# Kernel optimization log

Measured on AMD Instinct MI355X. Metric: run time of the kernel, lower is better.

Reference implementation:

```python
import jax, jax.numpy as jnp
import numpy as np

IN_V = 16
OUT_V = 16
HS = 64
INCR = 2
METRIC = jnp.array([1.0, -1.0, -1.0, -1.0], dtype=jnp.float32)


def setup_inputs() -> dict:
    key = jax.random.key(0)
    ks = jax.random.split(key, 9)
    B, N = 64, 1024
    vectors = jax.random.normal(ks[0], (B, N, IN_V, 4), dtype=jnp.float32)
    scalars = jax.random.normal(ks[1], (B, N, HS), dtype=jnp.float32)
    # kaiming-uniform-ish init scale for [out, in] weights
    def w(k, o, i):
        bound = 1.0 / np.sqrt(i)
        return jax.random.uniform(k, (o, i), jnp.float32, -bound, bound)
    Wq = w(ks[2], IN_V * INCR, IN_V)
    Wk = w(ks[3], IN_V * INCR, IN_V)
    Wv = w(ks[4], OUT_V, IN_V)  # exp() applied in forward (EquiLinearTimelike)
    Wq_s = w(ks[5], HS, HS)
    Wk_s = w(ks[6], HS, HS)
    bq_s = jax.random.uniform(ks[7], (HS,), jnp.float32, -1 / np.sqrt(HS), 1 / np.sqrt(HS))
    bk_s = jax.random.uniform(ks[8], (HS,), jnp.float32, -1 / np.sqrt(HS), 1 / np.sqrt(HS))
    return {"vectors": vectors, "scalars": scalars, "Wq": Wq, "Wq_s": Wq_s,
            "bq_s": bq_s, "Wk": Wk, "Wk_s": Wk_s, "bk_s": bk_s, "Wv": Wv}


def reference(vectors, scalars, Wq, Wq_s, bq_s, Wk, Wk_s, bk_s, Wv):
    B, N = vectors.shape[:2]
    # Lorentz squared norm: t^2 - x^2 - y^2 - z^2 over last axis -> [B,N,IN_V,1]
    norm = jnp.einsum('bnik,k->bni', vectors * vectors, METRIC)[..., None]
    vecs = vectors / jnp.sqrt(jnp.clip(jnp.abs(norm), 1e-5))
    # Q/K vector projections [B,N,IN_V*INCR,4] and scalar projections [B,N,HS]
    q_v = jnp.einsum('ij,bnjk->bnik', Wq, vecs)
    k_v = jnp.einsum('ij,bnjk->bnik', Wk, vecs)
    q_s = scalars @ Wq_s.T + bq_s
    k_s = scalars @ Wk_s.T + bk_s
    # embed: flatten vectors (K gets metric factor) and concat scalars
    q = jnp.concatenate([q_v.reshape(B, N, -1), q_s], axis=-1)
    k = jnp.concatenate([(k_v * METRIC).reshape(B, N, -1), k_s], axis=-1)
    # V: positive-weight (timelike) projection, flatten -> [B,N,OUT_V*4]
    v = jnp.einsum('ij,bnjk->bnik', jnp.exp(Wv), vecs).reshape(B, N, -1)
    # scaled dot-product attention over the particle axis
    scale = 1.0 / jnp.sqrt(jnp.asarray(q.shape[-1], q.dtype))
    scores = jnp.einsum('bqd,bkd->bqk', q, k) * scale
    attn = jax.nn.softmax(scores, axis=-1)
    out = jnp.einsum('bqk,bkd->bqd', attn, v)
    return out.reshape(B, N, -1, 4)
```

## Files before the change

kernel.cpp:

```cpp
#include <hip/hip_runtime.h>
#include <math.h>

typedef float f32x16 __attribute__((ext_vector_type(16)));
typedef short bf16x8 __attribute__((ext_vector_type(8)));
typedef short bf16x4 __attribute__((ext_vector_type(4)));
typedef unsigned short u16;
typedef unsigned int u32;

#define MFMA32(a, b, c) __builtin_amdgcn_mfma_f32_32x32x16_bf16(a, b, c, 0, 0, 0)

__device__ __forceinline__ u16 f2bf(float x) {
    u32 u = __float_as_uint(x);
    u += 0x7FFFu + ((u >> 16) & 1u);
    return (u16)(u >> 16);
}
__device__ __forceinline__ float bf2f(u16 h) {
    return __uint_as_float(((u32)h) << 16);
}
__device__ __forceinline__ void gload16(const void* g, void* l) {
    __builtin_amdgcn_global_load_lds(
        (const __attribute__((address_space(1))) unsigned int*)g,
        (__attribute__((address_space(3))) unsigned int*)l, 16, 0, 0);
}

__global__ __launch_bounds__(256) void g_kernel(
    const float* __restrict__ Wq, const float* __restrict__ Wk,
    const float* __restrict__ Wv,
    u16* __restrict__ gmh, u16* __restrict__ gml,
    u16* __restrict__ mvh, u16* __restrict__ mvl)
{
    const int bk = blockIdx.x;
    const int base = ((bk & 3) * 256 + threadIdx.x) * 4;
    if (bk < 4) {
#pragma unroll
        for (int i = 0; i < 4; ++i) {
            int e = base + i;
            int f = e >> 6, fp = e & 63;
            int c = f & 3, cp = fp & 3, j = f >> 2, jp = fp >> 2;
            float val = 0.f;
            if (c == cp) {
                float a0 = 0.f, a1 = 0.f;
#pragma unroll 8
                for (int ff = 0; ff < 32; ff += 2) {
                    a0 = fmaf(Wq[ff * 16 + j],       Wk[ff * 16 + jp],       a0);
                    a1 = fmaf(Wq[(ff + 1) * 16 + j], Wk[(ff + 1) * 16 + jp], a1);
                }
                val = (a0 + a1) * ((c == 0) ? 1.f : -1.f);
            }
            u16 h = f2bf(val);
            gmh[e] = h; gml[e] = f2bf(val - bf2f(h));
        }
    } else {
#pragma unroll
        for (int i = 0; i < 4; ++i) {
            int e = base + i;
            int f = e >> 6, fp = e & 63;
            float val = ((f & 3) == (fp & 3)) ? expf(Wv[(f >> 2) * 16 + (fp >> 2)]) : 0.f;
            u16 h = f2bf(val);
            mvh[e] = h; mvl[e] = f2bf(val - bf2f(h));
        }
    }
}

__global__ __launch_bounds__(256) void prep_kernel(
    const float* __restrict__ vectors, const float* __restrict__ scalars,
    const float* __restrict__ Wq_s, const float* __restrict__ bq_s,
    const float* __restrict__ Wk_s, const float* __restrict__ bk_s,
    const u16* __restrict__ gmh, const u16* __restrict__ gml,
    const u16* __restrict__ mvh, const u16* __restrict__ mvl,
    u16* __restrict__ qh, u16* __restrict__ ql,
    u16* __restrict__ kh, u16* __restrict__ kl,
    u16* __restrict__ vth)
{
    const int t = threadIdx.x;
    const int w = t >> 6;
    const int lane = t & 63;
    const int l31 = lane & 31, g = lane >> 5;
    const int b = blockIdx.x >> 5;
    const int n0 = (blockIdx.x & 31) << 5;
    const long tok0 = (long)b * 1024 + n0;
    const float SC2 = 0.07216878364870323f * 1.4426950408889634f;

    if (w == 1 || w == 2) {
        bf16x8 Ah[4], Al[4];
        const float* vrow = vectors + (tok0 + l31) * 64 + g * 8;
#pragma unroll
        for (int kk = 0; kk < 4; ++kk) {
            float4 x0 = *(const float4*)(vrow + kk * 16);
            float4 x1 = *(const float4*)(vrow + kk * 16 + 4);
            float nr0 = x0.x * x0.x - x0.y * x0.y - x0.z * x0.z - x0.w * x0.w;
            float iv0 = 1.0f / sqrtf(fmaxf(fabsf(nr0), 1e-5f));
            float nr1 = x1.x * x1.x - x1.y * x1.y - x1.z * x1.z - x1.w * x1.w;
            float iv1 = 1.0f / sqrtf(fmaxf(fabsf(nr1), 1e-5f));
            float xs[8] = {x0.x * iv0, x0.y * iv0, x0.z * iv0, x0.w * iv0,
                           x1.x * iv1, x1.y * iv1, x1.z * iv1, x1.w * iv1};
#pragma unroll
            for (int e = 0; e < 8; ++e) {
                u16 h = f2bf(xs[e]);
                Ah[kk][e] = (short)h;
                Al[kk][e] = (short)f2bf(xs[e] - bf2f(h));
            }
        }

        const u16* bhp = (w == 1) ? gmh : mvh;
        const u16* blp = (w == 1) ? gml : mvl;
#pragma unroll
        for (int tile = 0; tile < 2; ++tile) {
            const int fs = tile * 32 + l31;
            const u16* bh = bhp + fs * 64 + g * 8;
            const u16* bl = blp + fs * 64 + g * 8;
            f32x16 acc;
#pragma unroll
            for (int r = 0; r < 16; ++r) acc[r] = 0.f;
#pragma unroll
            for (int kk = 0; kk < 4; ++kk) {
                bf16x8 Bh = *(const bf16x8*)(bh + kk * 16);
                bf16x8 Bl = *(const bf16x8*)(bl + kk * 16);
                acc = MFMA32(Ah[kk], Bh, acc);
                acc = MFMA32(Al[kk], Bh, acc);
                acc = MFMA32(Ah[kk], Bl, acc);
            }
            if (w == 1) {
#pragma unroll
                for (int reg = 0; reg < 16; ++reg) {
                    int trow = (reg & 3) + 8 * (reg >> 2) + 4 * g;
                    float val = acc[reg];
                    u16 h = f2bf(val);
                    kh[(tok0 + trow) * 128 + fs] = h;
                    kl[(tok0 + trow) * 64 + fs] = f2bf(val - bf2f(h));
                }
            } else {
#pragma unroll
                for (int reg = 0; reg < 16; ++reg) {
                    int trow = (reg & 3) + 8 * (reg >> 2) + 4 * g;
                    vth[((long)b * 64 + fs) * 1024 + n0 + trow] = f2bf(acc[reg]);
                }
            }
        }
    } else {
        if (w == 0) {
            const float* vrow = vectors + (tok0 + l31) * 64 + g * 8;
#pragma unroll
            for (int kk = 0; kk < 4; ++kk) {
                float4 x0 = *(const float4*)(vrow + kk * 16);
                float4 x1 = *(const float4*)(vrow + kk * 16 + 4);
                float nr0 = x0.x * x0.x - x0.y * x0.y - x0.z * x0.z - x0.w * x0.w;
                float iv0 = SC2 / sqrtf(fmaxf(fabsf(nr0), 1e-5f));
                float nr1 = x1.x * x1.x - x1.y * x1.y - x1.z * x1.z - x1.w * x1.w;
                float iv1 = SC2 / sqrtf(fmaxf(fabsf(nr1), 1e-5f));
                float xs[8] = {x0.x * iv0, x0.y * iv0, x0.z * iv0, x0.w * iv0,
                               x1.x * iv1, x1.y * iv1, x1.z * iv1, x1.w * iv1};
                u16 hh[8], ll[8];
#pragma unroll
                for (int e = 0; e < 8; ++e) {
                    hh[e] = f2bf(xs[e]);
                    ll[e] = f2bf(xs[e] - bf2f(hh[e]));
                }
                *(int4*)(qh + (tok0 + l31) * 128 + kk * 16 + g * 8) = *(int4*)hh;
                *(int4*)(ql + (tok0 + l31) * 64 + kk * 16 + g * 8) = *(int4*)ll;
            }
        }
        const int isq = (w == 0);
        bf16x8 Ah[4];
        const float* xrow = scalars + (tok0 + l31) * 64 + g * 8;
#pragma unroll
        for (int kk = 0; kk < 4; ++kk) {
            float4 x0 = *(const float4*)(xrow + kk * 16);
            float4 x1 = *(const float4*)(xrow + kk * 16 + 4);
            float xs[8] = {x0.x, x0.y, x0.z, x0.w, x1.x, x1.y, x1.z, x1.w};
#pragma unroll
            for (int e = 0; e < 8; ++e) Ah[kk][e] = (short)f2bf(xs[e]);
        }
        const float sc = isq ? SC2 : 1.f;
        u16* oh = isq ? qh : kh;
#pragma unroll
        for (int ft = 0; ft < 2; ++ft) {
            const int fs = (ft << 5) + l31;
            const float* wrow = (isq ? Wq_s : Wk_s) + fs * 64 + g * 8;
            f32x16 acc;
#pragma unroll
            for (int r = 0; r < 16; ++r) acc[r] = 0.f;
#pragma unroll
            for (int kk = 0; kk < 4; ++kk) {
                float4 w0_ = *(const float4*)(wrow + kk * 16);
                float4 w1_ = *(const float4*)(wrow + kk * 16 + 4);
                float ws_[8] = {w0_.x, w0_.y, w0_.z, w0_.w, w1_.x, w1_.y, w1_.z, w1_.w};
                bf16x8 Bh;
#pragma unroll
                for (int e = 0; e < 8; ++e) Bh[e] = (short)f2bf(ws_[e]);
                acc = MFMA32(Ah[kk], Bh, acc);
            }
            const float bias = (isq ? bq_s : bk_s)[fs];
#pragma unroll
            for (int reg = 0; reg < 16; ++reg) {
                int trow = (reg & 3) + 8 * (reg >> 2) + 4 * g;
                oh[(tok0 + trow) * 128 + 64 + fs] = f2bf((acc[reg] + bias) * sc);
            }
        }
    }
}

__global__ __launch_bounds__(256) void attn_kernel(
    const u16* __restrict__ qh, const u16* __restrict__ ql,
    const u16* __restrict__ kh, const u16* __restrict__ kl,
    const u16* __restrict__ vth, float* __restrict__ out)
{
    __shared__ u16 KH[2 * 32 * 128];
    __shared__ u16 KL[2 * 32 * 64];
    __shared__ u16 VH[2 * 64 * 40];

    const int t = threadIdx.x;
    const int lane = t & 63;
    const int w = t >> 6;
    const int l31 = lane & 31, g = lane >> 5;

    const int bid = blockIdx.x;
    const int b = ((bid & 7) << 3) + (bid >> 6);
    const int qt = (bid >> 3) & 7;

    const int qi = qt * 128 + w * 32 + l31;
    const long qtok = (long)b * 1024 + qi;

    bf16x8 Qh[8], Qlv[4];
    {
        const u16* qhp = qh + qtok * 128 + g * 8;
        const u16* qlp = ql + qtok * 64 + g * 8;
#pragma unroll
        for (int c = 0; c < 8; ++c) Qh[c] = *(const bf16x8*)(qhp + c * 16);
#pragma unroll
        for (int c = 0; c < 4; ++c) Qlv[c] = *(const bf16x8*)(qlp + c * 16);
    }

    const int r0 = 8 * w + (lane >> 4);
    const int r1 = r0 + 4;
    const int su0 = (lane & 15) ^ (r0 & 15);
    const int su1 = (lane & 15) ^ (r1 & 15);
    const u16* kh0 = kh + ((long)b * 1024 + r0) * 128 + su0 * 8;
    const u16* kh1 = kh + ((long)b * 1024 + r1) * 128 + su1 * 8;
    const int rl_ = 8 * w + (lane >> 3);
    const int sul = (lane & 7) ^ (rl_ & 7);
    const u16* kl0 = kl + ((long)b * 1024 + rl_) * 64 + sul * 8;

    const int vdv = t >> 2, vq4 = t & 3;
    const u16* vhg = vth + ((long)b * 64 + vdv) * 1024 + vq4 * 8;
    u16* vdst = VH + vdv * 40 + vq4 * 8;
    int4 rv0;

#define STAGEK(kt, bf) do { \
        gload16(kh0 + (long)(kt) * 128, KH + (bf) * 4096 + w * 1024); \
        gload16(kh1 + (long)(kt) * 128, KH + (bf) * 4096 + w * 1024 + 512); \
        gload16(kl0 + (long)(kt) * 64,  KL + (bf) * 2048 + w * 512); \
    } while (0)

    f32x16 o0, o1;
#pragma unroll
    for (int r = 0; r < 16; ++r) { o0[r] = 0.f; o1[r] = 0.f; }
    float m_run = -1e30f, l_run = 0.f;

    rv0 = *(const int4*)(vhg);
    STAGEK(0, 0);
    *(int4*)(vdst) = rv0;
    __syncthreads();

#pragma unroll 2
    for (int it = 0; it < 32; ++it) {
        const int cb = it & 1;
        if (it < 31) {
            rv0 = *(const int4*)(vhg + (it + 1) * 32);
            STAGEK((it + 1) * 32, cb ^ 1);
        }

        f32x16 sA, sB;
#pragma unroll
        for (int r = 0; r < 16; ++r) { sA[r] = 0.f; sB[r] = 0.f; }
        const u16* kbh = KH + cb * 4096 + l31 * 128;
        const u16* kbl = KL + cb * 2048 + l31 * 64;
        const int rs = l31 & 15, rs7 = l31 & 7;
        __builtin_amdgcn_s_setprio(1);
#pragma unroll
        for (int c = 0; c < 4; ++c) {
            bf16x8 fh = *(const bf16x8*)(kbh + ((g + 2 * c) ^ rs) * 8);
            bf16x8 fl = *(const bf16x8*)(kbl + ((g + 2 * c) ^ rs7) * 8);
            sA = MFMA32(fh, Qh[c], sA);
            sB = MFMA32(fl, Qh[c], sB);
            sB = MFMA32(fh, Qlv[c], sB);
        }
#pragma unroll
        for (int c = 4; c < 8; ++c) {
            bf16x8 fh = *(const bf16x8*)(kbh + ((g + 2 * c) ^ rs) * 8);
            sA = MFMA32(fh, Qh[c], sA);
        }
        __builtin_amdgcn_s_setprio(0);

        float s[16];
#pragma unroll
        for (int r = 0; r < 16; ++r) s[r] = sA[r] + sB[r];
        float m01 = fmaxf(s[0], s[1]),   m23 = fmaxf(s[2], s[3]);
        float m45 = fmaxf(s[4], s[5]),   m67 = fmaxf(s[6], s[7]);
        float m89 = fmaxf(s[8], s[9]),   mab = fmaxf(s[10], s[11]);
        float mcd = fmaxf(s[12], s[13]), mef = fmaxf(s[14], s[15]);
        float mt = fmaxf(fmaxf(fmaxf(m01, m23), fmaxf(m45, m67)),
                         fmaxf(fmaxf(m89, mab), fmaxf(mcd, mef)));
        mt = fmaxf(mt, __shfl_xor(mt, 32));
        if (!__all(mt - m_run <= 11.54f)) {
            float mn = fmaxf(m_run, mt);
            float corr = __builtin_amdgcn_exp2f(m_run - mn);
            l_run *= corr;
#pragma unroll
            for (int r = 0; r < 16; ++r) { o0[r] *= corr; o1[r] *= corr; }
            m_run = mn;
        }
#pragma unroll
        for (int r = 0; r < 16; ++r) s[r] = __builtin_amdgcn_exp2f(s[r] - m_run);
        float p01 = s[0] + s[1],   p23 = s[2] + s[3];
        float p45 = s[4] + s[5],   p67 = s[6] + s[7];
        float p89 = s[8] + s[9],   pab = s[10] + s[11];
        float pcd = s[12] + s[13], pef = s[14] + s[15];
        float ps = ((p01 + p23) + (p45 + p67)) + ((p89 + pab) + (pcd + pef));
        ps += __shfl_xor(ps, 32);
        l_run += ps;

        u32 pk[4], pk2[4];
#pragma unroll
        for (int e = 0; e < 4; ++e) {
            pk[e]  = __builtin_amdgcn_perm(__float_as_uint(s[2 * e + 1]),
                                           __float_as_uint(s[2 * e]), 0x07060302u);
            pk2[e] = __builtin_amdgcn_perm(__float_as_uint(s[8 + 2 * e + 1]),
                                           __float_as_uint(s[8 + 2 * e]), 0x07060302u);
        }
        bf16x8 ph0 = *(bf16x8*)pk;
        bf16x8 ph1 = *(bf16x8*)pk2;

        const u16* vb = VH + cb * 2560;
        bf16x8 v00, v01, v10, v11;
        {
            const u16* p00 = vb + l31 * 40 + g * 4;
            const u16* p10 = vb + (32 + l31) * 40 + g * 4;
            bf16x4 a0 = *(const bf16x4*)(p00);      bf16x4 a1 = *(const bf16x4*)(p00 + 8);
            bf16x4 b0 = *(const bf16x4*)(p00 + 16); bf16x4 b1 = *(const bf16x4*)(p00 + 24);
            bf16x4 c0 = *(const bf16x4*)(p10);      bf16x4 c1 = *(const bf16x4*)(p10 + 8);
            bf16x4 d0 = *(const bf16x4*)(p10 + 16); bf16x4 d1 = *(const bf16x4*)(p10 + 24);
            v00 = __builtin_shufflevector(a0, a1, 0, 1, 2, 3, 4, 5, 6, 7);
            v01 = __builtin_shufflevector(b0, b1, 0, 1, 2, 3, 4, 5, 6, 7);
            v10 = __builtin_shufflevector(c0, c1, 0, 1, 2, 3, 4, 5, 6, 7);
            v11 = __builtin_shufflevector(d0, d1, 0, 1, 2, 3, 4, 5, 6, 7);
        }

        __builtin_amdgcn_s_setprio(1);
        o0 = MFMA32(v00, ph0, o0);
        o0 = MFMA32(v01, ph1, o0);
        o1 = MFMA32(v10, ph0, o1);
        o1 = MFMA32(v11, ph1, o1);
        __builtin_amdgcn_s_setprio(0);

        if (it < 31) *(int4*)(vdst + (cb ^ 1) * 2560) = rv0;
        __syncthreads();
    }

    float inv = 1.0f / l_run;
    float* op = out + qtok * 64;
#pragma unroll
    for (int sg = 0; sg < 4; ++sg) {
        *(float4*)(op + sg * 8 + g * 4) = make_float4(
            o0[4*sg+0]*inv, o0[4*sg+1]*inv, o0[4*sg+2]*inv, o0[4*sg+3]*inv);
        *(float4*)(op + 32 + sg * 8 + g * 4) = make_float4(
            o1[4*sg+0]*inv, o1[4*sg+1]*inv, o1[4*sg+2]*inv, o1[4*sg+3]*inv);
    }
#undef STAGEK
}

extern "C" void kernel_launch(void* const* d_in, const int* in_sizes, int n_in,
                              void* d_out, int out_size, void* d_ws, size_t ws_size,
                              hipStream_t stream) {
    const float* vectors = (const float*)d_in[0];
    const float* scalars = (const float*)d_in[1];
    const float* Wq   = (const float*)d_in[2];
    const float* Wq_s = (const float*)d_in[3];
    const float* bq_s = (const float*)d_in[4];
    const float* Wk   = (const float*)d_in[5];
    const float* Wk_s = (const float*)d_in[6];
    const float* bk_s = (const float*)d_in[7];
    const float* Wv   = (const float*)d_in[8];
    float* o = (float*)d_out;

    u16* qh  = (u16*)d_ws;
    u16* ql  = qh + 8388608;
    u16* kh  = ql + 4194304;
    u16* kl  = kh + 8388608;
    u16* vth = kl + 4194304;
    u16* gmh = vth + 4194304;
    u16* gml = gmh + 4096;
    u16* mvh = gml + 4096;
    u16* mvl = mvh + 4096;

    g_kernel<<<8, 256, 0, stream>>>(Wq, Wk, Wv, gmh, gml, mvh, mvl);
    prep_kernel<<<2048, 256, 0, stream>>>(vectors, scalars, Wq_s, bq_s,
                                          Wk_s, bk_s, gmh, gml, mvh, mvl,
                                          qh, ql, kh, kl, vth);
    attn_kernel<<<512, 256, 0, stream>>>(qh, ql, kh, kl, vth, o);
}
```

Baseline: 92.55 us.

## Defer P·V MFMAs one iteration to overlap them with QK MFMAs

The P·V matrix multiplies of each KV tile are delayed by one iteration and issued right after the next tile's QK MFMAs, with a final flush after the loop. This keeps the matrix unit busy while the softmax VALU work and exp computation run, instead of serialising softmax and P·V. Accumulation order stays correct because the deferred product is added before the next running-max rescale. The cost is extra live registers for the carried V and P fragments, which may lower occupancy, plus one extra MFMA block on zeros in the first iteration.

Result: no change. 92.85 us (+0.3%).

```diff
diff --git a/kernel.cpp b/kernel.cpp
--- a/kernel.cpp
+++ b/kernel.cpp
@@ -257,6 +257,13 @@
     for (int r = 0; r < 16; ++r) { o0[r] = 0.f; o1[r] = 0.f; }
     float m_run = -1e30f, l_run = 0.f;
 
+    bf16x8 vp00, vp01, vp10, vp11, php0, php1;
+#pragma unroll
+    for (int e = 0; e < 8; ++e) {
+        vp00[e] = 0; vp01[e] = 0; vp10[e] = 0; vp11[e] = 0;
+        php0[e] = 0; php1[e] = 0;
+    }
+
     rv0 = *(const int4*)(vhg);
     STAGEK(0, 0);
     *(int4*)(vdst) = rv0;
@@ -290,6 +297,10 @@
             bf16x8 fh = *(const bf16x8*)(kbh + ((g + 2 * c) ^ rs) * 8);
             sA = MFMA32(fh, Qh[c], sA);
         }
+        o0 = MFMA32(vp00, php0, o0);
+        o0 = MFMA32(vp01, php1, o0);
+        o1 = MFMA32(vp10, php0, o1);
+        o1 = MFMA32(vp11, php1, o1);
         __builtin_amdgcn_s_setprio(0);
 
         float s[16];
@@ -328,11 +339,10 @@
             pk2[e] = __builtin_amdgcn_perm(__float_as_uint(s[8 + 2 * e + 1]),
                                            __float_as_uint(s[8 + 2 * e]), 0x07060302u);
         }
-        bf16x8 ph0 = *(bf16x8*)pk;
-        bf16x8 ph1 = *(bf16x8*)pk2;
+        php0 = *(bf16x8*)pk;
+        php1 = *(bf16x8*)pk2;
 
         const u16* vb = VH + cb * 2560;
-        bf16x8 v00, v01, v10, v11;
         {
             const u16* p00 = vb + l31 * 40 + g * 4;
             const u16* p10 = vb + (32 + l31) * 40 + g * 4;
@@ -340,22 +350,22 @@
             bf16x4 b0 = *(const bf16x4*)(p00 + 16); bf16x4 b1 = *(const bf16x4*)(p00 + 24);
             bf16x4 c0 = *(const bf16x4*)(p10);      bf16x4 c1 = *(const bf16x4*)(p10 + 8);
             bf16x4 d0 = *(const bf16x4*)(p10 + 16); bf16x4 d1 = *(const bf16x4*)(p10 + 24);
-            v00 = __builtin_shufflevector(a0, a1, 0, 1, 2, 3, 4, 5, 6, 7);
-            v01 = __builtin_shufflevector(b0, b1, 0, 1, 2, 3, 4, 5, 6, 7);
-            v10 = __builtin_shufflevector(c0, c1, 0, 1, 2, 3, 4, 5, 6, 7);
-            v11 = __builtin_shufflevector(d0, d1, 0, 1, 2, 3, 4, 5, 6, 7);
-        }
-
-        __builtin_amdgcn_s_setprio(1);
-        o0 = MFMA32(v00, ph0, o0);
-        o0 = MFMA32(v01, ph1, o0);
-        o1 = MFMA32(v10, ph0, o1);
-        o1 = MFMA32(v11, ph1, o1);
-        __builtin_amdgcn_s_setprio(0);
+            vp00 = __builtin_shufflevector(a0, a1, 0, 1, 2, 3, 4, 5, 6, 7);
+            vp01 = __builtin_shufflevector(b0, b1, 0, 1, 2, 3, 4, 5, 6, 7);
+            vp10 = __builtin_shufflevector(c0, c1, 0, 1, 2, 3, 4, 5, 6, 7);
+            vp11 = __builtin_shufflevector(d0, d1, 0, 1, 2, 3, 4, 5, 6, 7);
+        }
 
         if (it < 31) *(int4*)(vdst + (cb ^ 1) * 2560) = rv0;
         __syncthreads();
     }
+
+    __builtin_amdgcn_s_setprio(1);
+    o0 = MFMA32(vp00, php0, o0);
+    o0 = MFMA32(vp01, php1, o0);
+    o1 = MFMA32(vp10, php0, o1);
+    o1 = MFMA32(vp11, php1, o1);
+    __builtin_amdgcn_s_setprio(0);
 
     float inv = 1.0f / l_run;
     float* op = out + qtok * 64;
```

## Switch attention K/V staging to four-buffer ring with one barrier per two tiles

Applied to the files above, without the earlier changes.

Grows the shared-memory K/V staging from double to quadruple buffering and processes two 32-key tiles per loop step, prefetching the next two tiles ahead. This halves the number of __syncthreads barriers and gives global loads more time to land before use. The cost is doubled LDS footprint (about 64KB per block), which may cut occupancy, plus extra VGPRs for two register-held V prefetches.

After: 94.00 us. About the same (+1.6%).

```diff
diff --git a/kernel.cpp b/kernel.cpp
--- a/kernel.cpp
+++ b/kernel.cpp
@@ -205,9 +205,9 @@
     const u16* __restrict__ kh, const u16* __restrict__ kl,
     const u16* __restrict__ vth, float* __restrict__ out)
 {
-    __shared__ u16 KH[2 * 32 * 128];
-    __shared__ u16 KL[2 * 32 * 64];
-    __shared__ u16 VH[2 * 64 * 40];
+    __shared__ u16 KH[4 * 32 * 128];
+    __shared__ u16 KL[4 * 32 * 64];
+    __shared__ u16 VH[4 * 64 * 40];
 
     const int t = threadIdx.x;
     const int lane = t & 63;
@@ -244,7 +244,7 @@
     const int vdv = t >> 2, vq4 = t & 3;
     const u16* vhg = vth + ((long)b * 64 + vdv) * 1024 + vq4 * 8;
     u16* vdst = VH + vdv * 40 + vq4 * 8;
-    int4 rv0;
+    int4 rvA, rvB;
 
 #define STAGEK(kt, bf) do { \
         gload16(kh0 + (long)(kt) * 128, KH + (bf) * 4096 + w * 1024); \
@@ -257,103 +257,117 @@
     for (int r = 0; r < 16; ++r) { o0[r] = 0.f; o1[r] = 0.f; }
     float m_run = -1e30f, l_run = 0.f;
 
-    rv0 = *(const int4*)(vhg);
+    rvA = *(const int4*)(vhg);
+    rvB = *(const int4*)(vhg + 32);
     STAGEK(0, 0);
-    *(int4*)(vdst) = rv0;
+    STAGEK(32, 1);
+    *(int4*)(vdst) = rvA;
+    *(int4*)(vdst + 2560) = rvB;
+    rvA = *(const int4*)(vhg + 64);
+    rvB = *(const int4*)(vhg + 96);
     __syncthreads();
 
-#pragma unroll 2
-    for (int it = 0; it < 32; ++it) {
-        const int cb = it & 1;
-        if (it < 31) {
-            rv0 = *(const int4*)(vhg + (it + 1) * 32);
-            STAGEK((it + 1) * 32, cb ^ 1);
-        }
-
-        f32x16 sA, sB;
-#pragma unroll
-        for (int r = 0; r < 16; ++r) { sA[r] = 0.f; sB[r] = 0.f; }
-        const u16* kbh = KH + cb * 4096 + l31 * 128;
-        const u16* kbl = KL + cb * 2048 + l31 * 64;
-        const int rs = l31 & 15, rs7 = l31 & 7;
-        __builtin_amdgcn_s_setprio(1);
-#pragma unroll
-        for (int c = 0; c < 4; ++c) {
-            bf16x8 fh = *(const bf16x8*)(kbh + ((g + 2 * c) ^ rs) * 8);
-            bf16x8 fl = *(const bf16x8*)(kbl + ((g + 2 * c) ^ rs7) * 8);
-            sA = MFMA32(fh, Qh[c], sA);
-            sB = MFMA32(fl, Qh[c], sB);
-            sB = MFMA32(fh, Qlv[c], sB);
-        }
-#pragma unroll
-        for (int c = 4; c < 8; ++c) {
-            bf16x8 fh = *(const bf16x8*)(kbh + ((g + 2 * c) ^ rs) * 8);
-            sA = MFMA32(fh, Qh[c], sA);
-        }
-        __builtin_amdgcn_s_setprio(0);
-
-        float s[16];
-#pragma unroll
-        for (int r = 0; r < 16; ++r) s[r] = sA[r] + sB[r];
-        float m01 = fmaxf(s[0], s[1]),   m23 = fmaxf(s[2], s[3]);
-        float m45 = fmaxf(s[4], s[5]),   m67 = fmaxf(s[6], s[7]);
-        float m89 = fmaxf(s[8], s[9]),   mab = fmaxf(s[10], s[11]);
-        float mcd = fmaxf(s[12], s[13]), mef = fmaxf(s[14], s[15]);
-        float mt = fmaxf(fmaxf(fmaxf(m01, m23), fmaxf(m45, m67)),
-                         fmaxf(fmaxf(m89, mab), fmaxf(mcd, mef)));
-        mt = fmaxf(mt, __shfl_xor(mt, 32));
-        if (!__all(mt - m_run <= 11.54f)) {
-            float mn = fmaxf(m_run, mt);
-            float corr = __builtin_amdgcn_exp2f(m_run - mn);
-            l_run *= corr;
-#pragma unroll
-            for (int r = 0; r < 16; ++r) { o0[r] *= corr; o1[r] *= corr; }
-            m_run = mn;
-        }
-#pragma unroll
-        for (int r = 0; r < 16; ++r) s[r] = __builtin_amdgcn_exp2f(s[r] - m_run);
-        float p01 = s[0] + s[1],   p23 = s[2] + s[3];
-        float p45 = s[4] + s[5],   p67 = s[6] + s[7];
-        float p89 = s[8] + s[9],   pab = s[10] + s[11];
-        float pcd = s[12] + s[13], pef = s[14] + s[15];
-        float ps = ((p01 + p23) + (p45 + p67)) + ((p89 + pab) + (pcd + pef));
-        ps += __shfl_xor(ps, 32);
-        l_run += ps;
-
-        u32 pk[4], pk2[4];
-#pragma unroll
-        for (int e = 0; e < 4; ++e) {
-            pk[e]  = __builtin_amdgcn_perm(__float_as_uint(s[2 * e + 1]),
-                                           __float_as_uint(s[2 * e]), 0x07060302u);
-            pk2[e] = __builtin_amdgcn_perm(__float_as_uint(s[8 + 2 * e + 1]),
-                                           __float_as_uint(s[8 + 2 * e]), 0x07060302u);
-        }
-        bf16x8 ph0 = *(bf16x8*)pk;
-        bf16x8 ph1 = *(bf16x8*)pk2;
-
-        const u16* vb = VH + cb * 2560;
-        bf16x8 v00, v01, v10, v11;
-        {
-            const u16* p00 = vb + l31 * 40 + g * 4;
-            const u16* p10 = vb + (32 + l31) * 40 + g * 4;
-            bf16x4 a0 = *(const bf16x4*)(p00);      bf16x4 a1 = *(const bf16x4*)(p00 + 8);
-            bf16x4 b0 = *(const bf16x4*)(p00 + 16); bf16x4 b1 = *(const bf16x4*)(p00 + 24);
-            bf16x4 c0 = *(const bf16x4*)(p10);      bf16x4 c1 = *(const bf16x4*)(p10 + 8);
-            bf16x4 d0 = *(const bf16x4*)(p10 + 16); bf16x4 d1 = *(const bf16x4*)(p10 + 24);
-            v00 = __builtin_shufflevector(a0, a1, 0, 1, 2, 3, 4, 5, 6, 7);
-            v01 = __builtin_shufflevector(b0, b1, 0, 1, 2, 3, 4, 5, 6, 7);
-            v10 = __builtin_shufflevector(c0, c1, 0, 1, 2, 3, 4, 5, 6, 7);
-            v11 = __builtin_shufflevector(d0, d1, 0, 1, 2, 3, 4, 5, 6, 7);
-        }
-
-        __builtin_amdgcn_s_setprio(1);
-        o0 = MFMA32(v00, ph0, o0);
-        o0 = MFMA32(v01, ph1, o0);
-        o1 = MFMA32(v10, ph0, o1);
-        o1 = MFMA32(v11, ph1, o1);
-        __builtin_amdgcn_s_setprio(0);
-
-        if (it < 31) *(int4*)(vdst + (cb ^ 1) * 2560) = rv0;
+    for (int p = 0; p < 16; ++p) {
+        if (p < 15) {
+            *(int4*)(vdst + ((2 * p + 2) & 3) * 2560) = rvA;
+            *(int4*)(vdst + ((2 * p + 3) & 3) * 2560) = rvB;
+            STAGEK((2 * p + 2) * 32, (2 * p + 2) & 3);
+            STAGEK((2 * p + 3) * 32, (2 * p + 3) & 3);
+            if (p < 14) {
+                rvA = *(const int4*)(vhg + (2 * p + 4) * 32);
+                rvB = *(const int4*)(vhg + (2 * p + 5) * 32);
+            }
+        }
+
+#pragma unroll
+        for (int h = 0; h < 2; ++h) {
+            const int it = 2 * p + h;
+            const int cb = it & 3;
+
+            f32x16 sA, sB;
+#pragma unroll
+            for (int r = 0; r < 16; ++r) { sA[r] = 0.f; sB[r] = 0.f; }
+            const u16* kbh = KH + cb * 4096 + l31 * 128;
+            const u16* kbl = KL + cb * 2048 + l31 * 64;
+            const int rs = l31 & 15, rs7 = l31 & 7;
+            __builtin_amdgcn_s_setprio(1);
+#pragma unroll
+            for (int c = 0; c < 4; ++c) {
+                bf16x8 fh = *(const bf16x8*)(kbh + ((g + 2 * c) ^ rs) * 8);
+                bf16x8 fl = *(const bf16x8*)(kbl + ((g + 2 * c) ^ rs7) * 8);
+                sA = MFMA32(fh, Qh[c], sA);
+                sB = MFMA32(fl, Qh[c], sB);
+                sB = MFMA32(fh, Qlv[c], sB);
+            }
+#pragma unroll
+            for (int c = 4; c < 8; ++c) {
+                bf16x8 fh = *(const bf16x8*)(kbh + ((g + 2 * c) ^ rs) * 8);
+                sA = MFMA32(fh, Qh[c], sA);
+            }
+            __builtin_amdgcn_s_setprio(0);
+
+            float s[16];
+#pragma unroll
+            for (int r = 0; r < 16; ++r) s[r] = sA[r] + sB[r];
+            float m01 = fmaxf(s[0], s[1]),   m23 = fmaxf(s[2], s[3]);
+            float m45 = fmaxf(s[4], s[5]),   m67 = fmaxf(s[6], s[7]);
+            float m89 = fmaxf(s[8], s[9]),   mab = fmaxf(s[10], s[11]);
+            float mcd = fmaxf(s[12], s[13]), mef = fmaxf(s[14], s[15]);
+            float mt = fmaxf(fmaxf(fmaxf(m01, m23), fmaxf(m45, m67)),
+                             fmaxf(fmaxf(m89, mab), fmaxf(mcd, mef)));
+            mt = fmaxf(mt, __shfl_xor(mt, 32));
+            if (!__all(mt - m_run <= 11.54f)) {
+                float mn = fmaxf(m_run, mt);
+                float corr = __builtin_amdgcn_exp2f(m_run - mn);
+                l_run *= corr;
+#pragma unroll
+                for (int r = 0; r < 16; ++r) { o0[r] *= corr; o1[r] *= corr; }
+                m_run = mn;
+            }
+#pragma unroll
+            for (int r = 0; r < 16; ++r) s[r] = __builtin_amdgcn_exp2f(s[r] - m_run);
+            float p01 = s[0] + s[1],   p23 = s[2] + s[3];
+            float p45 = s[4] + s[5],   p67 = s[6] + s[7];
+            float p89 = s[8] + s[9],   pab = s[10] + s[11];
+            float pcd = s[12] + s[13], pef = s[14] + s[15];
+            float ps = ((p01 + p23) + (p45 + p67)) + ((p89 + pab) + (pcd + pef));
+            ps += __shfl_xor(ps, 32);
+            l_run += ps;
+
+            u32 pk[4], pk2[4];
+#pragma unroll
+            for (int e = 0; e < 4; ++e) {
+                pk[e]  = __builtin_amdgcn_perm(__float_as_uint(s[2 * e + 1]),
+                                               __float_as_uint(s[2 * e]), 0x07060302u);
+                pk2[e] = __builtin_amdgcn_perm(__float_as_uint(s[8 + 2 * e + 1]),
+                                               __float_as_uint(s[8 + 2 * e]), 0x07060302u);
+            }
+            bf16x8 ph0 = *(bf16x8*)pk;
+            bf16x8 ph1 = *(bf16x8*)pk2;
+
+            const u16* vb = VH + cb * 2560;
+            bf16x8 v00, v01, v10, v11;
+            {
+                const u16* p00 = vb + l31 * 40 + g * 4;
+                const u16* p10 = vb + (32 + l31) * 40 + g * 4;
+                bf16x4 a0 = *(const bf16x4*)(p00);      bf16x4 a1 = *(const bf16x4*)(p00 + 8);
+                bf16x4 b0 = *(const bf16x4*)(p00 + 16); bf16x4 b1 = *(const bf16x4*)(p00 + 24);
+                bf16x4 c0 = *(const bf16x4*)(p10);      bf16x4 c1 = *(const bf16x4*)(p10 + 8);
+                bf16x4 d0 = *(const bf16x4*)(p10 + 16); bf16x4 d1 = *(const bf16x4*)(p10 + 24);
+                v00 = __builtin_shufflevector(a0, a1, 0, 1, 2, 3, 4, 5, 6, 7);
+                v01 = __builtin_shufflevector(b0, b1, 0, 1, 2, 3, 4, 5, 6, 7);
+                v10 = __builtin_shufflevector(c0, c1, 0, 1, 2, 3, 4, 5, 6, 7);
+                v11 = __builtin_shufflevector(d0, d1, 0, 1, 2, 3, 4, 5, 6, 7);
+            }
+
+            __builtin_amdgcn_s_setprio(1);
+            o0 = MFMA32(v00, ph0, o0);
+            o0 = MFMA32(v01, ph1, o0);
+            o1 = MFMA32(v10, ph0, o1);
+            o1 = MFMA32(v11, ph1, o1);
+            __builtin_amdgcn_s_setprio(0);
+        }
+
         __syncthreads();
     }
 
```
